# Performance work log

Measured on AMD Instinct MI355X. Metric: run time of the kernel, lower is better.

Reference implementation:

```python
import jax, jax.numpy as jnp
import numpy as np

S, B, I, H = 256, 512, 46, 256  # seqlen, batch, i_dim, h_dim
EPS = 1e-5


def setup_inputs() -> dict:
    key = jax.random.key(0)
    ks = iter(jax.random.split(key, 64))
    nrm = lambda shape, s=0.05: jax.random.normal(next(ks), shape, dtype=jnp.float32) * s
    inp = {}
    inp['X'] = jax.random.normal(next(ks), (S, B, I), dtype=jnp.float32)
    inp['M'] = (jax.random.uniform(next(ks), (S, B, I)) > 0.5).astype(jnp.float32)
    inp['mask'] = (jax.random.uniform(next(ks), (S, B)) > 0.1).astype(jnp.float32)
    C = I - 6  # 40 clinical channels
    inp['i2h_w'] = nrm((H, 6)); inp['i2h_b'] = nrm((H,))
    inp['comb_w'] = nrm((C, 2 * C)); inp['comb_b'] = nrm((C,))
    inp['down_w'] = nrm((H, C)); inp['down_b'] = nrm((H,))
    inp['conv1_w'] = nrm((H, C)); inp['conv1_b'] = nrm((H,))
    inp['conv2_w'] = nrm((H, H)); inp['conv2_b'] = nrm((H,))
    inp['bn1_g'] = jnp.ones((H,), jnp.float32); inp['bn1_b'] = jnp.zeros((H,), jnp.float32)
    inp['bn2_g'] = jnp.ones((H,), jnp.float32); inp['bn2_b'] = jnp.zeros((H,), jnp.float32)
    for p in ('r1', 'r2'):
        inp[p + '_wih'] = nrm((3 * H, H)); inp[p + '_whh'] = nrm((3 * H, H))
        inp[p + '_bih'] = nrm((3 * H,)); inp[p + '_bhh'] = nrm((3 * H,))
        inp[p + '_cw'] = nrm((H, 2 * H)); inp[p + '_cb'] = nrm((H,))
    inp['ln1_g'] = jnp.ones((H,), jnp.float32); inp['ln1_b'] = jnp.zeros((H,), jnp.float32)
    inp['ln2_g'] = jnp.ones((H,), jnp.float32); inp['ln2_b'] = jnp.zeros((H,), jnp.float32)
    inp['ln3_g'] = jnp.ones((8,), jnp.float32); inp['ln3_b'] = jnp.zeros((8,), jnp.float32)
    inp['nn1_w'] = nrm((8, H)); inp['nn1_b'] = nrm((8,))
    inp['nn2_w'] = nrm((2, 8)); inp['nn2_b'] = nrm((2,))
    return inp


def _bn(x, g, b):
    # BatchNorm1d in training mode: stats over (seq, batch) per channel, biased var
    mu = x.mean((0, 1))
    var = x.var((0, 1))
    return (x - mu) * jax.lax.rsqrt(var + EPS) * g + b


def _ln(x, g, b):
    mu = x.mean(-1, keepdims=True)
    var = x.var(-1, keepdims=True)
    return (x - mu) * jax.lax.rsqrt(var + EPS) * g + b


def _modgru(Xs, h0, mask, wih, whh, bih, bhh, cw, cb):
    # precompute input-gate projections for all timesteps: [S,B,3H]
    gi = jnp.einsum('sbi,gi->sbg', Xs, wih) + bih

    def step(h, inp):
        x, g, m = inp  # x:[B,H], g:[B,3H], m:[B]
        gh = h @ whh.T + bhh
        ir, iz, inn = jnp.split(g, 3, axis=-1)
        hr, hz, hn = jnp.split(gh, 3, axis=-1)
        r = jax.nn.sigmoid(ir + hr)
        z = jax.nn.sigmoid(iz + hz)
        n = jnp.tanh(inn + r * hn)
        h_new = (1.0 - z) * n + z * h  # GRUCell update
        mm = m[:, None]
        h = h_new * mm + h * (1.0 - mm)  # mask blend
        out = jnp.concatenate([x, h], axis=-1) @ cw.T + cb  # com2
        return h, out

    _, outs = jax.lax.scan(step, h0, (Xs, gi, mask))
    return outs


def reference(X, M, mask, i2h_w, i2h_b, comb_w, comb_b, down_w, down_b,
              conv1_w, conv1_b, conv2_w, conv2_b, bn1_g, bn1_b, bn2_g, bn2_b,
              r1_wih, r1_whh, r1_bih, r1_bhh, r1_cw, r1_cb,
              r2_wih, r2_whh, r2_bih, r2_bhh, r2_cw, r2_cb,
              ln1_g, ln1_b, ln2_g, ln2_b, ln3_g, ln3_b,
              nn1_w, nn1_b, nn2_w, nn2_b):
    p_info = X[0, :, -6:]          # [B,6] static patient info
    Xin = X[:, :, :-6]             # [S,B,40]
    Min = M[:, :, :-6]
    h0 = p_info @ i2h_w.T + i2h_b  # [B,H]
    res = Xin @ down_w.T + down_b  # [S,B,H]
    Xc = jnp.concatenate([Xin, Min], axis=-1) @ comb_w.T + comb_b
    # kernel-size-1 convs == per-timestep linear (layout kept [S,B,C])
    out = Xc @ conv1_w.T + conv1_b
    out = jax.nn.relu(_bn(out, bn1_g, bn1_b))
    out = out @ conv2_w.T + conv2_b
    out = _bn(out, bn2_g, bn2_b)
    hx = out + res
    hx = _ln(_modgru(hx, h0, mask, r1_wih, r1_whh, r1_bih, r1_bhh, r1_cw, r1_cb), ln1_g, ln1_b)
    hx = _ln(_modgru(hx, h0, mask, r2_wih, r2_whh, r2_bih, r2_bhh, r2_cw, r2_cb), ln2_g, ln2_b)
    hx = jax.nn.relu(hx @ nn1_w.T + nn1_b)
    hx = _ln(hx, ln3_g, ln3_b)
    return hx @ nn2_w.T + nn2_b  # [S,B,2]
```

## Files before the change

kernel.cpp:

```cpp
#include <hip/hip_runtime.h>
#include <hip/hip_bf16.h>

#define SS 256
#define BB 512
#define II 46
#define HH 256
#define CC 40
#define SB (SS*BB)
#define G3 (3*HH)
#define EPSF 1e-5f
#define NPART (SB/64)

typedef __attribute__((ext_vector_type(8))) short bf16x8;
typedef __attribute__((ext_vector_type(4))) float f32x4;

__device__ __forceinline__ unsigned short f2bf_rne(float f){
  unsigned u = __float_as_uint(f);
  unsigned r = (u + 0x7FFFu + ((u >> 16) & 1u)) >> 16;
  return (unsigned short)r;
}
__device__ __forceinline__ float bf2f(unsigned short b){
  return __uint_as_float(((unsigned)b) << 16);
}
__device__ __forceinline__ void cvt8(const float* v, bf16x8& hi, bf16x8& lo){
  #pragma unroll
  for (int e=0;e<8;e++){
    unsigned short hb = f2bf_rne(v[e]);
    hi[e] = (short)hb;
    lo[e] = (short)f2bf_rne(v[e] - bf2f(hb));
  }
}

__global__ void split_w_k(const float* __restrict__ w, unsigned short* __restrict__ wh,
                          unsigned short* __restrict__ wl, int n){
  int i = blockIdx.x*256 + threadIdx.x;
  if (i >= n) return;
  float v = w[i];
  unsigned short hb = f2bf_rne(v);
  wh[i] = hb;
  wl[i] = f2bf_rne(v - bf2f(hb));
}

__global__ void h0_k(const float* __restrict__ X, const float* __restrict__ w,
                     const float* __restrict__ bias, float* __restrict__ h1c,
                     float* __restrict__ h2c){
  int b = blockIdx.x, jj = threadIdx.x;
  const float* p = X + (long long)b*II + (II - 6);
  float acc = bias[jj];
  #pragma unroll
  for (int c2=0;c2<6;c2++) acc = fmaf(p[c2], w[jj*6 + c2], acc);
  h1c[(long long)b*HH + jj] = acc;
  h2c[(long long)b*HH + jj] = acc;
}

__global__ void wfrag_k(const float* __restrict__ whh, unsigned short* __restrict__ wf){
  int tid = blockIdx.x*256 + threadIdx.x;
  if (tid >= 384*64) return;
  int f = tid >> 6, l = tid & 63;
  int ntile = f >> 3, kt = f & 7;
  int col = ntile*16 + (l & 15);
  int k0  = kt*32 + (l >> 4)*8;
  unsigned short* dst = wf + (((size_t)f)*64 + l)*8;
  #pragma unroll
  for (int e=0;e<8;e++) dst[e] = f2bf_rne(whh[(size_t)col*HH + k0 + e]);
}

template<int MODE, int XM>
__global__ void gemm_tn(const float* __restrict__ A, int lda,
                        const float* __restrict__ W, int ldw,
                        const float* __restrict__ bias,
                        float* __restrict__ Co, int ldc,
                        int Mrows, int N, int K,
                        const float* __restrict__ A2, long long r0,
                        float* __restrict__ ps, float* __restrict__ pq, int pblk0)
{
  __shared__ __align__(16) float As[32][132];
  __shared__ __align__(16) float Ws[32][132];
  const int m0 = blockIdx.x*128, n0 = blockIdx.y*128;
  const int t  = threadIdx.x;
  const int tm = t >> 4, tn = t & 15;
  float acc[8][8];
  #pragma unroll
  for (int i=0;i<8;i++)
    #pragma unroll
    for (int j2=0;j2<8;j2++) acc[i][j2] = 0.f;

  for (int k0=0;k0<K;k0+=32){
    #pragma unroll
    for (int u=0;u<16;u++){
      int idx = u*256 + t;
      int r = idx >> 5, c = idx & 31;
      int gk = k0 + c;
      float av = 0.f, wv = 0.f;
      if (gk < K){
        int gm = m0 + r;
        if (gm < Mrows){
          if (XM){
            long long gr = r0 + gm;
            av = (gk < CC) ? A[gr*II + gk] : A2[gr*II + (gk - CC)];
          } else {
            av = A[(long long)gm*lda + gk];
          }
        }
        int gn = n0 + r;
        if (gn < N)     wv = W[(long long)gn*ldw + gk];
      }
      As[c][r] = av;
      Ws[c][r] = wv;
    }
    __syncthreads();
    #pragma unroll
    for (int kk=0;kk<32;kk++){
      const float4 a0 = *(const float4*)&As[kk][tm*8];
      const float4 a1 = *(const float4*)&As[kk][tm*8+4];
      const float4 b0 = *(const float4*)&Ws[kk][tn*8];
      const float4 b1 = *(const float4*)&Ws[kk][tn*8+4];
      const float av[8] = {a0.x,a0.y,a0.z,a0.w,a1.x,a1.y,a1.z,a1.w};
      const float bv[8] = {b0.x,b0.y,b0.z,b0.w,b1.x,b1.y,b1.z,b1.w};
      #pragma unroll
      for (int i=0;i<8;i++)
        #pragma unroll
        for (int j2=0;j2<8;j2++) acc[i][j2] = fmaf(av[i], bv[j2], acc[i][j2]);
    }
    __syncthreads();
  }

  if (MODE == 3){
    __shared__ float redS[16][128];
    __shared__ float redQ[16][128];
    #pragma unroll
    for (int j2=0;j2<8;j2++){
      const int gn = n0 + tn*8 + j2;
      const float bv = bias[gn];
      float s = 0.f, q = 0.f;
      #pragma unroll
      for (int i=0;i<8;i++){
        const float val = acc[i][j2] + bv;
        s += val; q = fmaf(val, val, q);
      }
      redS[tm][tn*8+j2] = s;
      redQ[tm][tn*8+j2] = q;
    }
    __syncthreads();
    if (t < 128){
      float ss = 0.f, qq = 0.f;
      #pragma unroll
      for (int m=0;m<16;m++){ ss += redS[m][t]; qq += redQ[m][t]; }
      ps[(size_t)(pblk0 + blockIdx.x)*HH + n0 + t] = ss;
      pq[(size_t)(pblk0 + blockIdx.x)*HH + n0 + t] = qq;
    }
    return;
  }

  const bool fullc = (n0 + 128 <= N);
  #pragma unroll
  for (int i=0;i<8;i++){
    int gm = m0 + tm*8 + i;
    if (gm < Mrows){
      if (fullc){
        float v[8];
        #pragma unroll
        for (int j2=0;j2<8;j2++){
          int gn = n0 + tn*8 + j2;
          float val = acc[i][j2] + bias[gn];
          if (MODE == 1) val = fmaxf(val, 0.f);
          v[j2] = val;
        }
        float* cp = &Co[(long long)gm*ldc + n0 + tn*8];
        if (MODE == 2){
          float4 o0 = *(float4*)cp, o1 = *(float4*)(cp+4);
          v[0]+=o0.x; v[1]+=o0.y; v[2]+=o0.z; v[3]+=o0.w;
          v[4]+=o1.x; v[5]+=o1.y; v[6]+=o1.z; v[7]+=o1.w;
        }
        *(float4*)cp     = make_float4(v[0],v[1],v[2],v[3]);
        *(float4*)(cp+4) = make_float4(v[4],v[5],v[6],v[7]);
      } else {
        #pragma unroll
        for (int j2=0;j2<8;j2++){
          int gn = n0 + tn*8 + j2;
          if (gn < N){
            long long oi = (long long)gm*ldc + gn;
            float val = acc[i][j2] + bias[gn];
            if (MODE == 1) val = fmaxf(val, 0.f);
            if (MODE == 2) val += Co[oi];
            Co[oi] = val;
          }
        }
      }
    }
  }
}

__global__ void gemm_tn_dual2(const float* __restrict__ Xb, long long r0,
                              const float* __restrict__ W1, const float* __restrict__ b1,
                              float* __restrict__ Co1,
                              const float* __restrict__ A2, const float* __restrict__ W2,
                              const float* __restrict__ b2, float* __restrict__ Co2,
                              int Mrows)
{
  __shared__ __align__(16) float As1[32][132];
  __shared__ __align__(16) float As2[32][132];
  __shared__ __align__(16) float Ws1[32][132];
  __shared__ __align__(16) float Ws2[32][132];
  const int m0 = blockIdx.x*128, n0 = blockIdx.y*128;
  const int t  = threadIdx.x;
  const int tm = t >> 4, tn = t & 15;
  float acc1[8][8], acc2[8][8];
  #pragma unroll
  for (int i=0;i<8;i++)
    #pragma unroll
    for (int j2=0;j2<8;j2++){ acc1[i][j2] = 0.f; acc2[i][j2] = 0.f; }

  for (int k0=0;k0<CC;k0+=32){
    #pragma unroll
    for (int u=0;u<16;u++){
      int idx = u*256 + t;
      int r = idx >> 5, c = idx & 31;
      int gk = k0 + c;
      float a1=0.f, a2=0.f, w1=0.f, w2=0.f;
      if (gk < CC){
        int gm = m0 + r;
        if (gm < Mrows){
          long long gr = r0 + gm;
          a1 = Xb[gr*II + gk];
          a2 = A2[(long long)gm*CC + gk];
        }
        int gn = n0 + r;
        w1 = W1[(long long)gn*CC + gk];
        w2 = W2[(long long)gn*CC + gk];
      }
      As1[c][r] = a1; As2[c][r] = a2;
      Ws1[c][r] = w1; Ws2[c][r] = w2;
    }
    __syncthreads();
    #pragma unroll
    for (int kk=0;kk<32;kk++){
      const float4 p0 = *(const float4*)&As1[kk][tm*8];
      const float4 p1 = *(const float4*)&As1[kk][tm*8+4];
      const float4 q0 = *(const float4*)&As2[kk][tm*8];
      const float4 q1 = *(const float4*)&As2[kk][tm*8+4];
      const float4 u0 = *(const float4*)&Ws1[kk][tn*8];
      const float4 u1 = *(const float4*)&Ws1[kk][tn*8+4];
      const float4 v0 = *(const float4*)&Ws2[kk][tn*8];
      const float4 v1 = *(const float4*)&Ws2[kk][tn*8+4];
      const float a1v[8] = {p0.x,p0.y,p0.z,p0.w,p1.x,p1.y,p1.z,p1.w};
      const float a2v[8] = {q0.x,q0.y,q0.z,q0.w,q1.x,q1.y,q1.z,q1.w};
      const float w1v[8] = {u0.x,u0.y,u0.z,u0.w,u1.x,u1.y,u1.z,u1.w};
      const float w2v[8] = {v0.x,v0.y,v0.z,v0.w,v1.x,v1.y,v1.z,v1.w};
      #pragma unroll
      for (int i=0;i<8;i++)
        #pragma unroll
        for (int j2=0;j2<8;j2++){
          acc1[i][j2] = fmaf(a1v[i], w1v[j2], acc1[i][j2]);
          acc2[i][j2] = fmaf(a2v[i], w2v[j2], acc2[i][j2]);
        }
    }
    __syncthreads();
  }
  #pragma unroll
  for (int i=0;i<8;i++){
    int gm = m0 + tm*8 + i;
    if (gm < Mrows){
      float v1[8], v2[8];
      #pragma unroll
      for (int j2=0;j2<8;j2++){
        int gn = n0 + tn*8 + j2;
        v1[j2] = acc1[i][j2] + b1[gn];
        v2[j2] = fmaxf(acc2[i][j2] + b2[gn], 0.f);
      }
      float* c1 = &Co1[(long long)gm*HH + n0 + tn*8];
      float* c2 = &Co2[(long long)gm*HH + n0 + tn*8];
      *(float4*)c1     = make_float4(v1[0],v1[1],v1[2],v1[3]);
      *(float4*)(c1+4) = make_float4(v1[4],v1[5],v1[6],v1[7]);
      *(float4*)c2     = make_float4(v2[0],v2[1],v2[2],v2[3]);
      *(float4*)(c2+4) = make_float4(v2[4],v2[5],v2[6],v2[7]);
    }
  }
}

template<int MODE>
__global__ __launch_bounds__(256) void gemm_mfp(
    const float* __restrict__ A, int lda,
    const unsigned short* __restrict__ Wh, const unsigned short* __restrict__ Wl, int ldw,
    const float* __restrict__ bias,
    float* __restrict__ Co, int ldc,
    int N, int K,
    float* __restrict__ ps, float* __restrict__ pq, int pblk0)
{
  __shared__ __align__(16) unsigned short Ah[128*32];
  __shared__ __align__(16) unsigned short Al[128*32];
  __shared__ __align__(16) unsigned short Bh[128*32];
  __shared__ __align__(16) unsigned short Bl[128*32];
  const int t = threadIdx.x;
  const int m0 = blockIdx.x*128, n0 = blockIdx.y*128;
  const int lane = t & 63, w = t >> 6;
  const int wm = (w & 1)*64, wn = (w >> 1)*64;
  const int fr = lane & 15, fg = lane >> 4;

  f32x4 acc[4][4];
  #pragma unroll
  for (int i=0;i<4;i++)
    #pragma unroll
    for (int j=0;j<4;j++){ f32x4 z; z[0]=0;z[1]=0;z[2]=0;z[3]=0; acc[i][j]=z; }

  for (int k0=0; k0<K; k0+=32){
    #pragma unroll
    for (int cc=0; cc<2; cc++){
      const int c   = t + cc*256;
      const int row = c >> 2, kg = c & 3;
      const int byte = row*64 + ((kg*16) ^ (((row>>1)&3)<<4));
      {
        const float* ap = A + (size_t)(m0+row)*lda + k0 + kg*8;
        float v[8];
        *(float4*)&v[0] = *(const float4*)ap;
        *(float4*)&v[4] = *(const float4*)(ap+4);
        bf16x8 hi, lo; cvt8(v, hi, lo);
        *(bf16x8*)((char*)Ah + byte) = hi;
        *(bf16x8*)((char*)Al + byte) = lo;
      }
      {
        const size_t off = (size_t)(n0+row)*ldw + k0 + kg*8;
        *(bf16x8*)((char*)Bh + byte) = *(const bf16x8*)&Wh[off];
        *(bf16x8*)((char*)Bl + byte) = *(const bf16x8*)&Wl[off];
      }
    }
    __syncthreads();
    bf16x8 ahi[4], alo[4], bhi[4], blo[4];
    #pragma unroll
    for (int mt=0; mt<4; mt++){
      const int r = wm + mt*16 + fr;
      const int byte = r*64 + ((fg*16) ^ (((r>>1)&3)<<4));
      ahi[mt] = *(const bf16x8*)((const char*)Ah + byte);
      alo[mt] = *(const bf16x8*)((const char*)Al + byte);
    }
    #pragma unroll
    for (int nt=0; nt<4; nt++){
      const int r = wn + nt*16 + fr;
      const int byte = r*64 + ((fg*16) ^ (((r>>1)&3)<<4));
      bhi[nt] = *(const bf16x8*)((const char*)Bh + byte);
      blo[nt] = *(const bf16x8*)((const char*)Bl + byte);
    }
    #pragma unroll
    for (int mt=0; mt<4; mt++)
      #pragma unroll
      for (int nt=0; nt<4; nt++){
        acc[mt][nt] = __builtin_amdgcn_mfma_f32_16x16x32_bf16(alo[mt], bhi[nt], acc[mt][nt], 0,0,0);
        acc[mt][nt] = __builtin_amdgcn_mfma_f32_16x16x32_bf16(ahi[mt], blo[nt], acc[mt][nt], 0,0,0);
        acc[mt][nt] = __builtin_amdgcn_mfma_f32_16x16x32_bf16(ahi[mt], bhi[nt], acc[mt][nt], 0,0,0);
      }
    __syncthreads();
  }

  if (MODE == 3){
    __shared__ float swS[4][4][16];
    __shared__ float qwS[4][4][16];
    float sv[4], qv[4];
    #pragma unroll
    for (int nt=0; nt<4; nt++){
      const int col = n0 + wn + nt*16 + fr;
      const float bv = bias[col];
      float s = 0.f, q = 0.f;
      #pragma unroll
      for (int mt=0; mt<4; mt++)
        #pragma unroll
        for (int i=0;i<4;i++){
          const float val = acc[mt][nt][i] + bv;
          s += val; q = fmaf(val, val, q);
        }
      s += __shfl_down(s, 32); q += __shfl_down(q, 32);
      s += __shfl_down(s, 16); q += __shfl_down(q, 16);
      sv[nt] = s; qv[nt] = q;
    }
    if (fg == 0){
      #pragma unroll
      for (int nt=0; nt<4; nt++){ swS[w][nt][fr] = sv[nt]; qwS[w][nt][fr] = qv[nt]; }
    }
    __syncthreads();
    if ((w & 1) == 0 && lane < 16){
      #pragma unroll
      for (int nt=0; nt<4; nt++){
        const int col = n0 + wn + nt*16 + fr;
        ps[(size_t)(pblk0 + blockIdx.x)*HH + col] = swS[w][nt][fr] + swS[w+1][nt][fr];
        pq[(size_t)(pblk0 + blockIdx.x)*HH + col] = qwS[w][nt][fr] + qwS[w+1][nt][fr];
      }
    }
    return;
  }

  #pragma unroll
  for (int mt=0; mt<4; mt++){
    #pragma unroll
    for (int nt=0; nt<4; nt++){
      const int col = n0 + wn + nt*16 + fr;
      const float bv = bias[col];
      #pragma unroll
      for (int i=0;i<4;i++){
        const int row = m0 + wm + mt*16 + fg*4 + i;
        const size_t oi = (size_t)row*ldc + col;
        float val = acc[mt][nt][i] + bv;
        if (MODE == 2) val += Co[oi];
        Co[oi] = val;
      }
    }
  }
}

__global__ __launch_bounds__(256) void gemm_mfp_dual(
    const float* __restrict__ A1, const float* __restrict__ A2,
    const unsigned short* __restrict__ Wh, const unsigned short* __restrict__ Wl,
    const float* __restrict__ bias,
    float* __restrict__ Co, int ldc, int N)
{
  __shared__ __align__(16) unsigned short Ah[128*32];
  __shared__ __align__(16) unsigned short Al[128*32];
  __shared__ __align__(16) unsigned short Bh[128*32];
  __shared__ __align__(16) unsigned short Bl[128*32];
  const int t = threadIdx.x;
  const int m0 = blockIdx.x*128, n0 = blockIdx.y*128;
  const int lane = t & 63, w = t >> 6;
  const int wm = (w & 1)*64, wn = (w >> 1)*64;
  const int fr = lane & 15, fg = lane >> 4;

  f32x4 acc[4][4];
  #pragma unroll
  for (int i=0;i<4;i++)
    #pragma unroll
    for (int j=0;j<4;j++){ f32x4 z; z[0]=0;z[1]=0;z[2]=0;z[3]=0; acc[i][j]=z; }

  for (int k0=0; k0<2*HH; k0+=32){
    const float* Abase = (k0 < HH) ? A1 : A2;
    const int    kofs  = (k0 < HH) ? k0 : (k0 - HH);
    #pragma unroll
    for (int cc=0; cc<2; cc++){
      const int c   = t + cc*256;
      const int row = c >> 2, kg = c & 3;
      const int byte = row*64 + ((kg*16) ^ (((row>>1)&3)<<4));
      {
        const float* ap = Abase + (size_t)(m0+row)*HH + kofs + kg*8;
        float v[8];
        *(float4*)&v[0] = *(const float4*)ap;
        *(float4*)&v[4] = *(const float4*)(ap+4);
        bf16x8 hi, lo; cvt8(v, hi, lo);
        *(bf16x8*)((char*)Ah + byte) = hi;
        *(bf16x8*)((char*)Al + byte) = lo;
      }
      {
        const size_t off = (size_t)(n0+row)*(2*HH) + k0 + kg*8;
        *(bf16x8*)((char*)Bh + byte) = *(const bf16x8*)&Wh[off];
        *(bf16x8*)((char*)Bl + byte) = *(const bf16x8*)&Wl[off];
      }
    }
    __syncthreads();
    bf16x8 ahi[4], alo[4], bhi[4], blo[4];
    #pragma unroll
    for (int mt=0; mt<4; mt++){
      const int r = wm + mt*16 + fr;
      const int byte = r*64 + ((fg*16) ^ (((r>>1)&3)<<4));
      ahi[mt] = *(const bf16x8*)((const char*)Ah + byte);
      alo[mt] = *(const bf16x8*)((const char*)Al + byte);
    }
    #pragma unroll
    for (int nt=0; nt<4; nt++){
      const int r = wn + nt*16 + fr;
      const int byte = r*64 + ((fg*16) ^ (((r>>1)&3)<<4));
      bhi[nt] = *(const bf16x8*)((const char*)Bh + byte);
      blo[nt] = *(const bf16x8*)((const char*)Bl + byte);
    }
    #pragma unroll
    for (int mt=0; mt<4; mt++)
      #pragma unroll
      for (int nt=0; nt<4; nt++){
        acc[mt][nt] = __builtin_amdgcn_mfma_f32_16x16x32_bf16(alo[mt], bhi[nt], acc[mt][nt], 0,0,0);
        acc[mt][nt] = __builtin_amdgcn_mfma_f32_16x16x32_bf16(ahi[mt], blo[nt], acc[mt][nt], 0,0,0);
        acc[mt][nt] = __builtin_amdgcn_mfma_f32_16x16x32_bf16(ahi[mt], bhi[nt], acc[mt][nt], 0,0,0);
      }
    __syncthreads();
  }

  #pragma unroll
  for (int mt=0; mt<4; mt++){
    #pragma unroll
    for (int nt=0; nt<4; nt++){
      const int col = n0 + wn + nt*16 + fr;
      const float bv = bias[col];
      #pragma unroll
      for (int i=0;i<4;i++){
        const int row = m0 + wm + mt*16 + fg*4 + i;
        const size_t oi = (size_t)row*ldc + col;
        Co[oi] = acc[mt][nt][i] + bv;
      }
    }
  }
}

__global__ void bn_final_k(const float* __restrict__ ps, const float* __restrict__ pq,
                           const float* __restrict__ g, const float* __restrict__ b,
                           float* __restrict__ sc, float* __restrict__ sh, int npart){
  const int col = blockIdx.x;
  const int t = threadIdx.x;
  double s = 0.0, q = 0.0;
  for (int i=t; i<npart; i+=256){
    s += (double)ps[(size_t)i*HH + col];
    q += (double)pq[(size_t)i*HH + col];
  }
  __shared__ double sd[256], qd[256];
  sd[t] = s; qd[t] = q;
  __syncthreads();
  for (int o=128;o>0;o>>=1){
    if (t < o){ sd[t] += sd[t+o]; qd[t] += qd[t+o]; }
    __syncthreads();
  }
  if (t == 0){
    double mu  = sd[0] / (double)SB;
    double var = qd[0] / (double)SB - mu*mu;
    float scv = (float)((double)g[col] / sqrt(var + 1e-5));
    sc[col] = scv;
    sh[col] = (float)((double)b[col] - mu*(double)scv);
  }
}

__global__ void fold_k(const float* __restrict__ w, const float* __restrict__ b,
                       const float* __restrict__ sc, const float* __restrict__ sh,
                       float* __restrict__ wf, float* __restrict__ bf, int K){
  int idx = blockIdx.x*blockDim.x + threadIdx.x;
  if (idx < 256*K){ int o = idx / K; wf[idx] = w[idx]*sc[o]; }
  if (idx < 256)  bf[idx] = b[idx]*sc[idx] + sh[idx];
}

__global__ void ln_rows_k(const float* __restrict__ Xi, float* __restrict__ Xo,
                          const float* __restrict__ g, const float* __restrict__ b){
  long long row = blockIdx.x;
  int t = threadIdx.x;
  float v = Xi[row*HH + t];
  float s = v, q = v*v;
  #pragma unroll
  for (int o=32;o>0;o>>=1){ s += __shfl_down(s,o); q += __shfl_down(q,o); }
  __shared__ float ssm[4], qqm[4];
  int w = t >> 6;
  if ((t & 63) == 0){ ssm[w] = s; qqm[w] = q; }
  __syncthreads();
  if (t == 0){ ssm[0] = ssm[0]+ssm[1]+ssm[2]+ssm[3]; qqm[0] = qqm[0]+qqm[1]+qqm[2]+qqm[3]; }
  __syncthreads();
  s = ssm[0]; q = qqm[0];
  float mu  = s * (1.f/HH);
  float var = q * (1.f/HH) - mu*mu;
  float rs  = rsqrtf(var + EPSF);
  Xo[row*HH + t] = (v - mu)*rs*g[t] + b[t];
}

__global__ __launch_bounds__(512) void gru_scan_mfma_k(
  const float* __restrict__ gi1, const unsigned short* __restrict__ wf1,
  const float* __restrict__ b1v, const float* __restrict__ m1v,
  float* __restrict__ hc1, float* __restrict__ Hh1o, int nst1,
  const float* __restrict__ gi2, const unsigned short* __restrict__ wf2,
  const float* __restrict__ b2v, const float* __restrict__ m2v,
  float* __restrict__ hc2, float* __restrict__ Hh2o, int nst2)
{
  const int gsel = blockIdx.x & 1;
  const int blk  = blockIdx.x >> 1;
  const float* gi    = gsel ? gi2 : gi1;
  const unsigned short* wfr = gsel ? wf2 : wf1;
  const float* bhh   = gsel ? b2v : b1v;
  const float* mask0 = gsel ? m2v : m1v;
  float* hcar        = gsel ? hc2 : hc1;
  float* Hh          = gsel ? Hh2o : Hh1o;
  const int nst      = gsel ? nst2 : nst1;
  if (nst <= 0) return;

  const int t    = threadIdx.x;
  const int b0   = blk*4;
  const int lane = t & 63, wid = t >> 6;
  const int arow = lane & 15, kg = lane >> 4;
  const bool act = (arow < 4);
  const int uj = t & 255, ur = t >> 8;

  __shared__ __align__(16) unsigned short AhS[4][256];
  __shared__ __align__(16) unsigned short AlS[4][256];
  __shared__ __align__(16) float ghS[4][768];
  __shared__ float mkz[4];

  float hold0 = hcar[(size_t)(b0+ur  )*HH + uj];
  float hold1 = hcar[(size_t)(b0+ur+2)*HH + uj];
  const float br = bhh[uj], bz = bhh[uj+HH], bn_ = bhh[uj+2*HH];

  {
    unsigned short hb0 = f2bf_rne(hold0);
    AhS[ur  ][uj] = hb0;  AlS[ur  ][uj] = f2bf_rne(hold0 - bf2f(hb0));
    unsigned short hb1 = f2bf_rne(hold1);
    AhS[ur+2][uj] = hb1;  AlS[ur+2][uj] = f2bf_rne(hold1 - bf2f(hb1));
  }
  __syncthreads();

  const unsigned short* wfbase = wfr + (((size_t)(wid*6)*8)*64 + lane)*8;

  for (int st=0; st<nst; ++st){
    const size_t ga = ((size_t)st*BB + b0 + ur  )*G3 + uj;
    const size_t gb = ((size_t)st*BB + b0 + ur+2)*G3 + uj;
    const float i0r=gi[ga], i0z=gi[ga+HH], i0n=gi[ga+2*HH];
    const float i1r=gi[gb], i1z=gi[gb+HH], i1n=gi[gb+2*HH];
    if (t < 4) mkz[t] = mask0[(size_t)st*BB + b0 + t];

    bf16x8 AH[8], AL[8];
    #pragma unroll
    for (int kt=0; kt<8; kt++){
      if (act){
        AH[kt] = *(const bf16x8*)&AhS[arow][kt*32 + kg*8];
        AL[kt] = *(const bf16x8*)&AlS[arow][kt*32 + kg*8];
      } else {
        bf16x8 z = {0,0,0,0,0,0,0,0};
        AH[kt] = z; AL[kt] = z;
      }
    }
    #pragma unroll
    for (int nt=0; nt<6; nt++){
      const unsigned short* wp = wfbase + (size_t)nt*8*64*8;
      f32x4 acc = {0.f,0.f,0.f,0.f};
      #pragma unroll
      for (int kt=0; kt<8; kt++){
        const bf16x8 b = *(const bf16x8*)(wp + (size_t)kt*64*8);
        acc = __builtin_amdgcn_mfma_f32_16x16x32_bf16(AL[kt], b, acc, 0,0,0);
        acc = __builtin_amdgcn_mfma_f32_16x16x32_bf16(AH[kt], b, acc, 0,0,0);
      }
      if (lane < 16){
        const int col = (wid*6 + nt)*16 + lane;
        ghS[0][col] = acc[0];
        ghS[1][col] = acc[1];
        ghS[2][col] = acc[2];
        ghS[3][col] = acc[3];
      }
    }
    __syncthreads();

    {
      const float ar = ghS[ur][uj]       + br;
      const float az = ghS[ur][uj+HH]    + bz;
      const float an = ghS[ur][uj+2*HH]  + bn_;
      const float rr = 1.f/(1.f + __expf(-(i0r + ar)));
      const float zz = 1.f/(1.f + __expf(-(i0z + az)));
      const float nn = tanhf(fmaf(rr, an, i0n));
      const float m  = mkz[ur];
      const float hnew = (1.f - zz)*nn + zz*hold0;
      const float hv = hnew*m + hold0*(1.f - m);
      hold0 = hv;
      unsigned short hb = f2bf_rne(hv);
      AhS[ur][uj] = hb; AlS[ur][uj] = f2bf_rne(hv - bf2f(hb));
      Hh[((size_t)st*BB + b0 + ur)*HH + uj] = hv;
    }
    {
      const int r_ = ur + 2;
      const float ar = ghS[r_][uj]       + br;
      const float az = ghS[r_][uj+HH]    + bz;
      const float an = ghS[r_][uj+2*HH]  + bn_;
      const float rr = 1.f/(1.f + __expf(-(i1r + ar)));
      const float zz = 1.f/(1.f + __expf(-(i1z + az)));
      const float nn = tanhf(fmaf(rr, an, i1n));
      const float m  = mkz[r_];
      const float hnew = (1.f - zz)*nn + zz*hold1;
      const float hv = hnew*m + hold1*(1.f - m);
      hold1 = hv;
      unsigned short hb = f2bf_rne(hv);
      AhS[r_][uj] = hb; AlS[r_][uj] = f2bf_rne(hv - bf2f(hb));
      Hh[((size_t)st*BB + b0 + r_)*HH + uj] = hv;
    }
    __syncthreads();
  }
  hcar[(size_t)(b0+ur  )*HH + uj] = hold0;
  hcar[(size_t)(b0+ur+2)*HH + uj] = hold1;
}

__global__ void head_ln_k(const float* __restrict__ hx,
                          const float* __restrict__ g2, const float* __restrict__ b2,
                          const float* __restrict__ w1, const float* __restrict__ b1,
                          const float* __restrict__ g3, const float* __restrict__ b3,
                          const float* __restrict__ w2, const float* __restrict__ b2h,
                          float* __restrict__ outp, long long r0){
  long long row = blockIdx.x;
  int t = threadIdx.x;
  float v = hx[row*HH + t];
  float s = v, q = v*v;
  #pragma unroll
  for (int o=32;o>0;o>>=1){ s += __shfl_down(s,o); q += __shfl_down(q,o); }
  __shared__ float ssm[4], qqm[4];
  int w = t >> 6;
  if ((t & 63) == 0){ ssm[w] = s; qqm[w] = q; }
  __syncthreads();
  if (t == 0){ ssm[0] = ssm[0]+ssm[1]+ssm[2]+ssm[3]; qqm[0] = qqm[0]+qqm[1]+qqm[2]+qqm[3]; }
  __syncthreads();
  s = ssm[0]; q = qqm[0];
  float mu  = s * (1.f/HH);
  float var = q * (1.f/HH) - mu*mu;
  float rs  = rsqrtf(var + EPSF);
  __shared__ float xs[HH];
  xs[t] = (v - mu)*rs*g2[t] + b2[t];
  __syncthreads();
  int o = t >> 5, l = t & 31;
  const float* wv = w1 + o*HH;
  float acc = 0.f;
  for (int k=l;k<HH;k+=32) acc = fmaf(xs[k], wv[k], acc);
  #pragma unroll
  for (int d=16;d>0;d>>=1) acc += __shfl_down(acc, d, 32);
  __shared__ float a8[8];
  if (l == 0) a8[o] = fmaxf(acc + b1[o], 0.f);
  __syncthreads();
  if (t == 0){
    float ss = 0.f;
    #pragma unroll
    for (int i=0;i<8;i++) ss += a8[i];
    float m8 = ss*0.125f;
    float qq = 0.f;
    #pragma unroll
    for (int i=0;i<8;i++){ float d = a8[i]-m8; qq = fmaf(d,d,qq); }
    float r8 = rsqrtf(qq*0.125f + EPSF);
    float y0 = b2h[0], y1 = b2h[1];
    #pragma unroll
    for (int i=0;i<8;i++){
      float vv = (a8[i]-m8)*r8*g3[i] + b3[i];
      y0 = fmaf(vv, w2[i],   y0);
      y1 = fmaf(vv, w2[8+i], y1);
    }
    outp[(r0+row)*2+0] = y0; outp[(r0+row)*2+1] = y1;
  }
}

extern "C" void kernel_launch(void* const* d_in, const int* in_sizes, int n_in,
                              void* d_out, int out_size, void* d_ws, size_t ws_size,
                              hipStream_t stream) {
  const float* X      = (const float*)d_in[0];
  const float* Mi     = (const float*)d_in[1];
  const float* mask   = (const float*)d_in[2];
  const float* i2h_w  = (const float*)d_in[3];
  const float* i2h_b  = (const float*)d_in[4];
  const float* comb_w = (const float*)d_in[5];
  const float* comb_b = (const float*)d_in[6];
  const float* down_w = (const float*)d_in[7];
  const float* down_b = (const float*)d_in[8];
  const float* conv1_w= (const float*)d_in[9];
  const float* conv1_b= (const float*)d_in[10];
  const float* conv2_w= (const float*)d_in[11];
  const float* conv2_b= (const float*)d_in[12];
  const float* bn1_g  = (const float*)d_in[13];
  const float* bn1_b  = (const float*)d_in[14];
  const float* bn2_g  = (const float*)d_in[15];
  const float* bn2_b  = (const float*)d_in[16];
  const float* r1_wih = (const float*)d_in[17];
  const float* r1_whh = (const float*)d_in[18];
  const float* r1_bih = (const float*)d_in[19];
  const float* r1_bhh = (const float*)d_in[20];
  const float* r1_cw  = (const float*)d_in[21];
  const float* r1_cb  = (const float*)d_in[22];
  const float* r2_wih = (const float*)d_in[23];
  const float* r2_whh = (const float*)d_in[24];
  const float* r2_bih = (const float*)d_in[25];
  const float* r2_bhh = (const float*)d_in[26];
  const float* r2_cw  = (const float*)d_in[27];
  const float* r2_cb  = (const float*)d_in[28];
  const float* ln1_g  = (const float*)d_in[29];
  const float* ln1_b  = (const float*)d_in[30];
  const float* ln2_g  = (const float*)d_in[31];
  const float* ln2_b  = (const float*)d_in[32];
  const float* ln3_g  = (const float*)d_in[33];
  const float* ln3_b  = (const float*)d_in[34];
  const float* nn1_w  = (const float*)d_in[35];
  const float* nn1_b  = (const float*)d_in[36];
  const float* nn2_w  = (const float*)d_in[37];
  const float* nn2_b  = (const float*)d_in[38];
  float* outp = (float*)d_out;

  const size_t us_elems = 2*((size_t)HH*HH + (size_t)HH*HH + (size_t)G3*HH
                           + (size_t)G3*HH + (size_t)HH*2*HH + (size_t)HH*2*HH)
                        + 2*(size_t)G3*HH;
  const size_t tail_floats = 2*(size_t)BB*HH + 2*(size_t)NPART*HH + 2*HH
                           + (size_t)256*40 + 256 + (size_t)HH*HH + 256
                           + (size_t)SB*CC
                           + (us_elems + 1)/2;
  int cands[6] = {256,128,64,32,16,8};
  int sc_chunk = 0;
  for (int ci=0; ci<6; ci++){
    size_t R = (size_t)512*cands[ci];
    size_t need = (R*2560 + tail_floats)*sizeof(float);
    if (need <= ws_size && R*2560 >= (size_t)SB*HH){ sc_chunk = cands[ci]; break; }
  }
  if (!sc_chunk) return;

  const size_t R = (size_t)512*sc_chunk;
  const int Ri = (int)R;
  const int nchunks = SB / Ri;

  float* wsf = (float*)d_ws;
  float* A   = wsf;
  float* GI1 = A + R*HH;
  float* Cxp = GI1;
  float* GI2 = GI1 + R*G3;
  float* Ee  = GI2 + R*G3;
  float* Hh2 = Ee + R*HH;
  float* Hx1 = Hh2 + R*HH;
  float* tl  = Hx1 + R*HH;
  float* H1C = tl;
  float* H2C = H1C + (size_t)BB*HH;
  float* PS  = H2C + (size_t)BB*HH;
  float* PQ  = PS  + (size_t)NPART*HH;
  float* SCv = PQ  + (size_t)NPART*HH;
  float* SHv = SCv + HH;
  float* W1F = SHv + HH;
  float* B1F = W1F + (size_t)256*40;
  float* W2F = B1F + HH;
  float* B2F = W2F + (size_t)HH*HH;
  float* XcF = B2F + HH;
  unsigned short* usb = (unsigned short*)(XcF + (size_t)SB*CC);
  unsigned short* C2H  = usb;
  unsigned short* C2L  = C2H  + (size_t)HH*HH;
  unsigned short* W2FH = C2L  + (size_t)HH*HH;
  unsigned short* W2FL = W2FH + (size_t)HH*HH;
  unsigned short* WI1H = W2FL + (size_t)HH*HH;
  unsigned short* WI1L = WI1H + (size_t)G3*HH;
  unsigned short* WI2H = WI1L + (size_t)G3*HH;
  unsigned short* WI2L = WI2H + (size_t)G3*HH;
  unsigned short* CW1H = WI2L + (size_t)G3*HH;
  unsigned short* CW1L = CW1H + (size_t)HH*2*HH;
  unsigned short* CW2H = CW1L + (size_t)HH*2*HH;
  unsigned short* CW2L = CW2H + (size_t)HH*2*HH;
  unsigned short* WF1  = CW2L + (size_t)HH*2*HH;
  unsigned short* WF2  = WF1 + (size_t)G3*HH;

  wfrag_k<<<(384*64 + 255)/256, 256, 0, stream>>>(r1_whh, WF1);
  wfrag_k<<<(384*64 + 255)/256, 256, 0, stream>>>(r2_whh, WF2);
  split_w_k<<<(HH*HH + 255)/256, 256, 0, stream>>>(conv2_w, C2H, C2L, HH*HH);
  split_w_k<<<(G3*HH + 255)/256, 256, 0, stream>>>(r1_wih, WI1H, WI1L, G3*HH);
  split_w_k<<<(G3*HH + 255)/256, 256, 0, stream>>>(r2_wih, WI2H, WI2L, G3*HH);
  split_w_k<<<(HH*2*HH + 255)/256, 256, 0, stream>>>(r1_cw, CW1H, CW1L, HH*2*HH);
  split_w_k<<<(HH*2*HH + 255)/256, 256, 0, stream>>>(r2_cw, CW2H, CW2L, HH*2*HH);

  const int MB = Ri/128;

  gemm_tn<0,1><<<dim3(SB/128,1), 256, 0, stream>>>(X, II, comb_w, 80, comb_b, XcF, CC, SB, CC, 80, Mi, 0, nullptr, nullptr, 0);
  gemm_tn<3,0><<<dim3(SB/128,2), 256, 0, stream>>>(XcF, CC, conv1_w, CC, conv1_b, nullptr, 0, SB, HH, CC, nullptr, 0, PS, PQ, 0);
  bn_final_k<<<256, 256, 0, stream>>>(PS, PQ, bn1_g, bn1_b, SCv, SHv, SB/128);
  fold_k<<<(256*40 + 255)/256, 256, 0, stream>>>(conv1_w, conv1_b, SCv, SHv, W1F, B1F, 40);

  {
    float* SA2 = wsf;
    for (int hlf=0; hlf<2; hlf++){
      long long r0 = (long long)hlf*(SB/2);
      gemm_tn<1,0><<<dim3(SB/256,2), 256, 0, stream>>>(XcF + r0*CC, CC, W1F, CC, B1F, SA2, HH, SB/2, HH, CC, nullptr, 0, nullptr, nullptr, 0);
      gemm_mfp<3><<<dim3(SB/256,2), 256, 0, stream>>>(SA2, HH, C2H, C2L, HH, conv2_b, nullptr, 0, HH, HH, PS, PQ, hlf*(SB/256));
    }
  }
  bn_final_k<<<256, 256, 0, stream>>>(PS, PQ, bn2_g, bn2_b, SCv, SHv, 2*(SB/256));
  fold_k<<<(256*256 + 255)/256, 256, 0, stream>>>(conv2_w, conv2_b, SCv, SHv, W2F, B2F, 256);
  split_w_k<<<(HH*HH + 255)/256, 256, 0, stream>>>(W2F, W2FH, W2FL, HH*HH);

  h0_k<<<BB, HH, 0, stream>>>(X, i2h_w, i2h_b, H1C, H2C);

  for (int c=0;c<nchunks;c++){
    long long r0 = (long long)c*R;
    long long rp = r0 - (long long)R;
    gemm_tn_dual2<<<dim3(MB,2), 256, 0, stream>>>(X, r0, down_w, down_b, A,
                                                  XcF + r0*CC, W1F, B1F, Ee, Ri);
    gemm_mfp<2><<<dim3(MB,2), 256, 0, stream>>>(Ee, HH, W2FH, W2FL, HH, B2F, A, HH, HH, HH, nullptr, nullptr, 0);
    gemm_mfp<0><<<dim3(MB,6), 256, 0, stream>>>(A, HH, WI1H, WI1L, HH, r1_bih, GI1, G3, G3, HH, nullptr, nullptr, 0);
    gru_scan_mfma_k<<<2*(BB/4), 512, 0, stream>>>(
        GI1, WF1, r1_bhh, mask + r0, H1C, Ee, sc_chunk,
        GI2, WF2, r2_bhh, (c > 0) ? (mask + rp) : mask, H2C, Hh2, (c > 0) ? sc_chunk : 0);
    if (c > 0){
      gemm_mfp_dual<<<dim3(MB,2), 256, 0, stream>>>(Hx1, Hh2, CW2H, CW2L, r2_cb, Cxp, HH, HH);
      head_ln_k<<<Ri, 256, 0, stream>>>(Cxp, ln2_g, ln2_b, nn1_w, nn1_b, ln3_g, ln3_b, nn2_w, nn2_b, outp, rp);
    }
    gemm_mfp_dual<<<dim3(MB,2), 256, 0, stream>>>(A, Ee, CW1H, CW1L, r1_cb, Cxp, HH, HH);
    ln_rows_k<<<Ri, 256, 0, stream>>>(Cxp, Hx1, ln1_g, ln1_b);
    gemm_mfp<0><<<dim3(MB,6), 256, 0, stream>>>(Hx1, HH, WI2H, WI2L, HH, r2_bih, GI2, G3, G3, HH, nullptr, nullptr, 0);
  }
  {
    long long rl = (long long)(nchunks-1)*R;
    gru_scan_mfma_k<<<2*(BB/4), 512, 0, stream>>>(
        GI1, WF1, r1_bhh, mask, H1C, Ee, 0,
        GI2, WF2, r2_bhh, mask + rl, H2C, Hh2, sc_chunk);
    gemm_mfp_dual<<<dim3(MB,2), 256, 0, stream>>>(Hx1, Hh2, CW2H, CW2L, r2_cb, Cxp, HH, HH);
    head_ln_k<<<Ri, 256, 0, stream>>>(Cxp, ln2_g, ln2_b, nn1_w, nn1_b, ln3_g, ln3_b, nn2_w, nn2_b, outp, rl);
  }
}
```

Baseline: 5.521 ms.

## Fuse conv1 recompute into conv2 BN-stats GEMM, drop intermediate buffer

Replaces the two-pass conv1 GEMM plus MFMA stats GEMM with one kernel. It recomputes the folded conv1+ReLU activations on the fly from Xc staged in shared memory and feeds them straight into the bf16-split MFMA conv2 GEMM that accumulates BN2 statistics. This removes writing and re-reading the large SB×H intermediate activation. Because that buffer is gone, the workspace chunk-size check no longer requires room for it, which may permit smaller chunks. The cost is redundant scalar FMA work: each N-block recomputes the 40-wide dot products, using scalar shared-memory reads.

```diff
diff --git a/kernel.cpp b/kernel.cpp
--- a/kernel.cpp
+++ b/kernel.cpp
@@ -278,14 +278,128 @@
   }
 }
 
+__global__ __launch_bounds__(256) void conv2stats_k(
+    const float* __restrict__ Xc,
+    const float* __restrict__ W1F,
+    const float* __restrict__ B1F,
+    const unsigned short* __restrict__ Wh, const unsigned short* __restrict__ Wl,
+    const float* __restrict__ bias,
+    float* __restrict__ ps, float* __restrict__ pq)
+{
+  __shared__ __align__(16) float Xs[40][132];
+  __shared__ __align__(16) unsigned short Ah[128*32];
+  __shared__ __align__(16) unsigned short Al[128*32];
+  __shared__ __align__(16) unsigned short Bh[128*32];
+  __shared__ __align__(16) unsigned short Bl[128*32];
+  const int t = threadIdx.x;
+  const int m0 = blockIdx.x*128, n0 = blockIdx.y*128;
+  const int lane = t & 63, w = t >> 6;
+  const int wm = (w & 1)*64, wn = (w >> 1)*64;
+  const int fr = lane & 15, fg = lane >> 4;
+
+  for (int idx = t; idx < 128*CC; idx += 256){
+    int r = idx / CC, k = idx - r*CC;
+    Xs[k][r] = Xc[(size_t)(m0 + r)*CC + k];
+  }
+  __syncthreads();
+
+  f32x4 acc[4][4];
+  #pragma unroll
+  for (int i=0;i<4;i++)
+    #pragma unroll
+    for (int j=0;j<4;j++){ f32x4 z; z[0]=0;z[1]=0;z[2]=0;z[3]=0; acc[i][j]=z; }
+
+  for (int k0=0; k0<HH; k0+=32){
+    #pragma unroll
+    for (int cc=0; cc<2; cc++){
+      const int c   = t + cc*256;
+      const int row = c >> 2, kg = c & 3;
+      float v[8];
+      #pragma unroll
+      for (int e=0;e<8;e++){
+        const int col = k0 + kg*8 + e;
+        const float* wp = W1F + (size_t)col*CC;
+        float a = 0.f;
+        #pragma unroll
+        for (int k=0;k<CC;k++) a = fmaf(Xs[k][row], wp[k], a);
+        v[e] = fmaxf(a + B1F[col], 0.f);
+      }
+      bf16x8 hi, lo; cvt8(v, hi, lo);
+      const int byte = row*64 + ((kg*16) ^ (((row>>1)&3)<<4));
+      *(bf16x8*)((char*)Ah + byte) = hi;
+      *(bf16x8*)((char*)Al + byte) = lo;
+      const size_t off = (size_t)(n0+row)*HH + k0 + kg*8;
+      *(bf16x8*)((char*)Bh + byte) = *(const bf16x8*)&Wh[off];
+      *(bf16x8*)((char*)Bl + byte) = *(const bf16x8*)&Wl[off];
+    }
+    __syncthreads();
+    bf16x8 ahi[4], alo[4], bhi[4], blo[4];
+    #pragma unroll
+    for (int mt=0; mt<4; mt++){
+      const int r = wm + mt*16 + fr;
+      const int byte = r*64 + ((fg*16) ^ (((r>>1)&3)<<4));
+      ahi[mt] = *(const bf16x8*)((const char*)Ah + byte);
+      alo[mt] = *(const bf16x8*)((const char*)Al + byte);
+    }
+    #pragma unroll
+    for (int nt=0; nt<4; nt++){
+      const int r = wn + nt*16 + fr;
+      const int byte = r*64 + ((fg*16) ^ (((r>>1)&3)<<4));
+      bhi[nt] = *(const bf16x8*)((const char*)Bh + byte);
+      blo[nt] = *(const bf16x8*)((const char*)Bl + byte);
+    }
+    #pragma unroll
+    for (int mt=0; mt<4; mt++)
+      #pragma unroll
+      for (int nt=0; nt<4; nt++){
+        acc[mt][nt] = __builtin_amdgcn_mfma_f32_16x16x32_bf16(alo[mt], bhi[nt], acc[mt][nt], 0,0,0);
+        acc[mt][nt] = __builtin_amdgcn_mfma_f32_16x16x32_bf16(ahi[mt], blo[nt], acc[mt][nt], 0,0,0);
+        acc[mt][nt] = __builtin_amdgcn_mfma_f32_16x16x32_bf16(ahi[mt], bhi[nt], acc[mt][nt], 0,0,0);
+      }
+    __syncthreads();
+  }
+
+  __shared__ float swS[4][4][16];
+  __shared__ float qwS[4][4][16];
+  float sv[4], qv[4];
+  #pragma unroll
+  for (int nt=0; nt<4; nt++){
+    const int col = n0 + wn + nt*16 + fr;
+    const float bv = bias[col];
+    float s = 0.f, q = 0.f;
+    #pragma unroll
+    for (int mt=0; mt<4; mt++)
+      #pragma unroll
+      for (int i=0;i<4;i++){
+        const float val = acc[mt][nt][i] + bv;
+        s += val; q = fmaf(val, val, q);
+      }
+    s += __shfl_down(s, 32); q += __shfl_down(q, 32);
+    s += __shfl_down(s, 16); q += __shfl_down(q, 16);
+    sv[nt] = s; qv[nt] = q;
+  }
+  if (fg == 0){
+    #pragma unroll
+    for (int nt=0; nt<4; nt++){ swS[w][nt][fr] = sv[nt]; qwS[w][nt][fr] = qv[nt]; }
+  }
+  __syncthreads();
+  if ((w & 1) == 0 && lane < 16){
+    #pragma unroll
+    for (int nt=0; nt<4; nt++){
+      const int col = n0 + wn + nt*16 + fr;
+      ps[(size_t)blockIdx.x*HH + col] = swS[w][nt][fr] + swS[w+1][nt][fr];
+      pq[(size_t)blockIdx.x*HH + col] = qwS[w][nt][fr] + qwS[w+1][nt][fr];
+    }
+  }
+}
+
 template<int MODE>
 __global__ __launch_bounds__(256) void gemm_mfp(
     const float* __restrict__ A, int lda,
     const unsigned short* __restrict__ Wh, const unsigned short* __restrict__ Wl, int ldw,
     const float* __restrict__ bias,
     float* __restrict__ Co, int ldc,
-    int N, int K,
-    float* __restrict__ ps, float* __restrict__ pq, int pblk0)
+    int N, int K)
 {
   __shared__ __align__(16) unsigned short Ah[128*32];
   __shared__ __align__(16) unsigned short Al[128*32];
@@ -349,42 +463,6 @@
         acc[mt][nt] = __builtin_amdgcn_mfma_f32_16x16x32_bf16(ahi[mt], bhi[nt], acc[mt][nt], 0,0,0);
       }
     __syncthreads();
-  }
-
-  if (MODE == 3){
-    __shared__ float swS[4][4][16];
-    __shared__ float qwS[4][4][16];
-    float sv[4], qv[4];
-    #pragma unroll
-    for (int nt=0; nt<4; nt++){
-      const int col = n0 + wn + nt*16 + fr;
-      const float bv = bias[col];
-      float s = 0.f, q = 0.f;
-      #pragma unroll
-      for (int mt=0; mt<4; mt++)
-        #pragma unroll
-        for (int i=0;i<4;i++){
-          const float val = acc[mt][nt][i] + bv;
-          s += val; q = fmaf(val, val, q);
-        }
-      s += __shfl_down(s, 32); q += __shfl_down(q, 32);
-      s += __shfl_down(s, 16); q += __shfl_down(q, 16);
-      sv[nt] = s; qv[nt] = q;
-    }
-    if (fg == 0){
-      #pragma unroll
-      for (int nt=0; nt<4; nt++){ swS[w][nt][fr] = sv[nt]; qwS[w][nt][fr] = qv[nt]; }
-    }
-    __syncthreads();
-    if ((w & 1) == 0 && lane < 16){
-      #pragma unroll
-      for (int nt=0; nt<4; nt++){
-        const int col = n0 + wn + nt*16 + fr;
-        ps[(size_t)(pblk0 + blockIdx.x)*HH + col] = swS[w][nt][fr] + swS[w+1][nt][fr];
-        pq[(size_t)(pblk0 + blockIdx.x)*HH + col] = qwS[w][nt][fr] + qwS[w+1][nt][fr];
-      }
-    }
-    return;
   }
 
   #pragma unroll
@@ -778,7 +856,7 @@
   for (int ci=0; ci<6; ci++){
     size_t R = (size_t)512*cands[ci];
     size_t need = (R*2560 + tail_floats)*sizeof(float);
-    if (need <= ws_size && R*2560 >= (size_t)SB*HH){ sc_chunk = cands[ci]; break; }
+    if (need <= ws_size){ sc_chunk = cands[ci]; break; }
   }
   if (!sc_chunk) return;
 
@@ -837,15 +915,8 @@
   bn_final_k<<<256, 256, 0, stream>>>(PS, PQ, bn1_g, bn1_b, SCv, SHv, SB/128);
   fold_k<<<(256*40 + 255)/256, 256, 0, stream>>>(conv1_w, conv1_b, SCv, SHv, W1F, B1F, 40);
 
-  {
-    float* SA2 = wsf;
-    for (int hlf=0; hlf<2; hlf++){
-      long long r0 = (long long)hlf*(SB/2);
-      gemm_tn<1,0><<<dim3(SB/256,2), 256, 0, stream>>>(XcF + r0*CC, CC, W1F, CC, B1F, SA2, HH, SB/2, HH, CC, nullptr, 0, nullptr, nullptr, 0);
-      gemm_mfp<3><<<dim3(SB/256,2), 256, 0, stream>>>(SA2, HH, C2H, C2L, HH, conv2_b, nullptr, 0, HH, HH, PS, PQ, hlf*(SB/256));
-    }
-  }
-  bn_final_k<<<256, 256, 0, stream>>>(PS, PQ, bn2_g, bn2_b, SCv, SHv, 2*(SB/256));
+  conv2stats_k<<<dim3(SB/128, 2), 256, 0, stream>>>(XcF, W1F, B1F, C2H, C2L, conv2_b, PS, PQ);
+  bn_final_k<<<256, 256, 0, stream>>>(PS, PQ, bn2_g, bn2_b, SCv, SHv, SB/128);
   fold_k<<<(256*256 + 255)/256, 256, 0, stream>>>(conv2_w, conv2_b, SCv, SHv, W2F, B2F, 256);
   split_w_k<<<(HH*HH + 255)/256, 256, 0, stream>>>(W2F, W2FH, W2FL, HH*HH);
 
@@ -856,8 +927,8 @@
     long long rp = r0 - (long long)R;
     gemm_tn_dual2<<<dim3(MB,2), 256, 0, stream>>>(X, r0, down_w, down_b, A,
                                                   XcF + r0*CC, W1F, B1F, Ee, Ri);
-    gemm_mfp<2><<<dim3(MB,2), 256, 0, stream>>>(Ee, HH, W2FH, W2FL, HH, B2F, A, HH, HH, HH, nullptr, nullptr, 0);
-    gemm_mfp<0><<<dim3(MB,6), 256, 0, stream>>>(A, HH, WI1H, WI1L, HH, r1_bih, GI1, G3, G3, HH, nullptr, nullptr, 0);
+    gemm_mfp<2><<<dim3(MB,2), 256, 0, stream>>>(Ee, HH, W2FH, W2FL, HH, B2F, A, HH, HH, HH);
+    gemm_mfp<0><<<dim3(MB,6), 256, 0, stream>>>(A, HH, WI1H, WI1L, HH, r1_bih, GI1, G3, G3, HH);
     gru_scan_mfma_k<<<2*(BB/4), 512, 0, stream>>>(
         GI1, WF1, r1_bhh, mask + r0, H1C, Ee, sc_chunk,
         GI2, WF2, r2_bhh, (c > 0) ? (mask + rp) : mask, H2C, Hh2, (c > 0) ? sc_chunk : 0);
@@ -867,7 +938,7 @@
     }
     gemm_mfp_dual<<<dim3(MB,2), 256, 0, stream>>>(A, Ee, CW1H, CW1L, r1_cb, Cxp, HH, HH);
     ln_rows_k<<<Ri, 256, 0, stream>>>(Cxp, Hx1, ln1_g, ln1_b);
-    gemm_mfp<0><<<dim3(MB,6), 256, 0, stream>>>(Hx1, HH, WI2H, WI2L, HH, r2_bih, GI2, G3, G3, HH, nullptr, nullptr, 0);
+    gemm_mfp<0><<<dim3(MB,6), 256, 0, stream>>>(Hx1, HH, WI2H, WI2L, HH, r2_bih, GI2, G3, G3, HH);
   }
   {
     long long rl = (long long)(nchunks-1)*R;
```

Measured after the change: 7.561 ms. 36.9% more time.
